# Kernel optimization log

Measured on AMD Instinct MI355X. Metric: run time of the kernel, lower is better.

The kernel has to match this reference:

```python
import jax, jax.numpy as jnp
import numpy as np

HIDDEN = 2048
NUM_EXPERTS = 64
TOP_K = 2
LOAD_BALANCE_ALPHA = 0.01
Z_LOSS_ALPHA = 1e-4
TEMPERATURE = 1.0  # buffer init, clamped to [0.1, 2.0] -> 1.0


def setup_inputs() -> dict:
    key = jax.random.key(0)
    k1, k2 = jax.random.split(key)
    x = jax.random.normal(k1, (4, 4096, HIDDEN), dtype=jnp.float32)
    W = jax.random.normal(k2, (NUM_EXPERTS, HIDDEN), dtype=jnp.float32) * (1.0 / np.sqrt(HIDDEN))
    return {"x": x, "W": W}


def reference(x, W):
    # Eval-mode forward of RuchbahMoEGate.
    B, S, H = x.shape
    x_flat = x.reshape(-1, H)                       # [N, H], N = B*S
    logits = jnp.einsum('nh,eh->ne', x_flat, W)     # gate projection, [N, E]
    logits = logits / TEMPERATURE                   # temp clamped to [0.1,2.0]
    scores = jax.nn.softmax(logits, axis=-1)        # [N, E]
    # top-k routing (eval: dynamic top-k == top_k, no capacity limitation)
    top_scores, top_idx = jax.lax.top_k(scores, TOP_K)   # [N, K]
    top_scores = jax.nn.softmax(top_scores.astype(jnp.float32), axis=-1).astype(x.dtype)
    # load-balance loss (eval: total_routing_count == 0 -> basic term only)
    expert_load = scores.mean(axis=0)               # [E]
    ideal_load = 1.0 / NUM_EXPERTS
    lb_loss = LOAD_BALANCE_ALPHA * jnp.sum((expert_load - ideal_load) ** 2)
    # z-loss: penalize large logit logsumexp
    z_loss = Z_LOSS_ALPHA * jnp.mean(jax.nn.logsumexp(logits, axis=-1) ** 2)
    total_loss = lb_loss + z_loss
    return top_scores, top_idx, total_loss
```

## Files before the change

kernel.cpp:

```cpp
#include <hip/hip_runtime.h>
#include <cstdint>
#include <cstddef>

#define HDIM 2048
#define NEXP 64
#define HC   16
#define BTOK 128
#define GTHR 128
#define PX   132
#define PW   68
#define GATE_TOK 16

__global__ __launch_bounds__(GTHR) void moe_gemm(const float* __restrict__ x,
                                                 const float* __restrict__ W,
                                                 float* __restrict__ partial,
                                                 int N, int HS) {
  __shared__ __align__(16) float xt[2][HC][PX];
  __shared__ __align__(16) float wt[2][HC][PW];

  const int ntb   = N / BTOK;
  const int tb    = blockIdx.x % ntb;
  const int hsIdx = blockIdx.x / ntb;
  const int tok0  = tb * BTOK;
  const int h0    = hsIdx * HS;
  const int tid   = threadIdx.x;
  const int lane  = tid & 63;
  const int wid   = tid >> 6;
  const int xoff  = wid * 64 + (lane >> 3) * 8;
  const int e0    = (lane & 7) * 8;
  const int srow  = tid >> 2;
  const int sj    = (tid & 3) * 4;

  float acc[8][8];
#pragma unroll
  for (int t = 0; t < 8; ++t)
#pragma unroll
    for (int e = 0; e < 8; ++e) acc[t][e] = 0.f;

  float4 xr[4], wr[2];

#pragma unroll
  for (int i = 0; i < 4; ++i)
    xr[i] = *reinterpret_cast<const float4*>(&x[(size_t)(tok0 + srow + i * 32) * HDIM + h0 + sj]);
#pragma unroll
  for (int i = 0; i < 2; ++i)
    wr[i] = *reinterpret_cast<const float4*>(&W[(size_t)(srow + i * 32) * HDIM + h0 + sj]);
#pragma unroll
  for (int i = 0; i < 4; ++i) {
    const int r = srow + i * 32;
    xt[0][sj + 0][r] = xr[i].x; xt[0][sj + 1][r] = xr[i].y;
    xt[0][sj + 2][r] = xr[i].z; xt[0][sj + 3][r] = xr[i].w;
  }
#pragma unroll
  for (int i = 0; i < 2; ++i) {
    const int r = srow + i * 32;
    wt[0][sj + 0][r] = wr[i].x; wt[0][sj + 1][r] = wr[i].y;
    wt[0][sj + 2][r] = wr[i].z; wt[0][sj + 3][r] = wr[i].w;
  }
  __syncthreads();

  const int niter = HS / HC;
  int cur = 0;
  for (int c = 0; c < niter; ++c) {
    if (c + 1 < niter) {
      const int hb = h0 + (c + 1) * HC;
#pragma unroll
      for (int i = 0; i < 4; ++i)
        xr[i] = *reinterpret_cast<const float4*>(&x[(size_t)(tok0 + srow + i * 32) * HDIM + hb + sj]);
#pragma unroll
      for (int i = 0; i < 2; ++i)
        wr[i] = *reinterpret_cast<const float4*>(&W[(size_t)(srow + i * 32) * HDIM + hb + sj]);
    }
#pragma unroll
    for (int h = 0; h < HC; ++h) {
      const float4 a0 = *reinterpret_cast<const float4*>(&xt[cur][h][xoff]);
      const float4 a1 = *reinterpret_cast<const float4*>(&xt[cur][h][xoff + 4]);
      const float4 b0 = *reinterpret_cast<const float4*>(&wt[cur][h][e0]);
      const float4 b1 = *reinterpret_cast<const float4*>(&wt[cur][h][e0 + 4]);
      const float xs[8] = {a0.x, a0.y, a0.z, a0.w, a1.x, a1.y, a1.z, a1.w};
      const float wv[8] = {b0.x, b0.y, b0.z, b0.w, b1.x, b1.y, b1.z, b1.w};
#pragma unroll
      for (int t = 0; t < 8; ++t)
#pragma unroll
        for (int e = 0; e < 8; ++e)
          acc[t][e] = fmaf(xs[t], wv[e], acc[t][e]);
    }
    if (c + 1 < niter) {
      const int nx = cur ^ 1;
#pragma unroll
      for (int i = 0; i < 4; ++i) {
        const int r = srow + i * 32;
        xt[nx][sj + 0][r] = xr[i].x; xt[nx][sj + 1][r] = xr[i].y;
        xt[nx][sj + 2][r] = xr[i].z; xt[nx][sj + 3][r] = xr[i].w;
      }
#pragma unroll
      for (int i = 0; i < 2; ++i) {
        const int r = srow + i * 32;
        wt[nx][sj + 0][r] = wr[i].x; wt[nx][sj + 1][r] = wr[i].y;
        wt[nx][sj + 2][r] = wr[i].z; wt[nx][sj + 3][r] = wr[i].w;
      }
    }
    __syncthreads();
    cur ^= 1;
  }

  const size_t base = ((size_t)hsIdx * N + (tok0 + xoff)) * NEXP + e0;
#pragma unroll
  for (int t = 0; t < 8; ++t) {
    *reinterpret_cast<float4*>(&partial[base + (size_t)t * NEXP]) =
        make_float4(acc[t][0], acc[t][1], acc[t][2], acc[t][3]);
    *reinterpret_cast<float4*>(&partial[base + (size_t)t * NEXP + 4]) =
        make_float4(acc[t][4], acc[t][5], acc[t][6], acc[t][7]);
  }
}

template <int HSPLIT>
__global__ __launch_bounds__(256) void moe_gate(const float* __restrict__ partial,
                                                int N,
                                                float* __restrict__ outS,
                                                float* __restrict__ outI,
                                                float* __restrict__ esumP,
                                                float* __restrict__ lse2P) {
  __shared__ float es[4][NEXP];
  __shared__ float l2[4];
  const int tid  = threadIdx.x;
  const int lane = tid & 63;
  const int w    = tid >> 6;
  const int base = blockIdx.x * GATE_TOK + w * 4;

  float esum = 0.f, lse2 = 0.f;
#pragma unroll
  for (int tt = 0; tt < 4; ++tt) {
    const int t = base + tt;
    float logit = 0.f;
#pragma unroll
    for (int hs = 0; hs < HSPLIT; ++hs)
      logit += partial[((size_t)hs * N + t) * NEXP + lane];

    float m = logit;
#pragma unroll
    for (int d = 1; d < 64; d <<= 1) m = fmaxf(m, __shfl_xor(m, d));
    const float p = expf(logit - m);
    float s = p;
#pragma unroll
    for (int d = 1; d < 64; d <<= 1) s += __shfl_xor(s, d);
    const float score = p / s;

    float v1 = score; int i1 = lane;
#pragma unroll
    for (int d = 1; d < 64; d <<= 1) {
      const float pv = __shfl_xor(v1, d);
      const int   pi = __shfl_xor(i1, d);
      if (pv > v1 || (pv == v1 && pi < i1)) { v1 = pv; i1 = pi; }
    }
    float v2 = (lane == i1) ? -1.f : score; int i2 = lane;
#pragma unroll
    for (int d = 1; d < 64; d <<= 1) {
      const float pv = __shfl_xor(v2, d);
      const int   pi = __shfl_xor(i2, d);
      if (pv > v2 || (pv == v2 && pi < i2)) { v2 = pv; i2 = pi; }
    }

    if (lane == 0) {
      const float mx  = fmaxf(v1, v2);
      const float e1  = expf(v1 - mx), e2 = expf(v2 - mx);
      const float inv = 1.f / (e1 + e2);
      *reinterpret_cast<float2*>(&outS[2 * (size_t)t]) = make_float2(e1 * inv, e2 * inv);
      *reinterpret_cast<float2*>(&outI[2 * (size_t)t]) = make_float2((float)i1, (float)i2);
    }

    esum += score;
    const float lse = m + logf(s);
    lse2 += lse * lse;
  }

  es[w][lane] = esum;
  if (lane == 0) l2[w] = lse2;
  __syncthreads();
  if (tid < NEXP)
    esumP[(size_t)blockIdx.x * NEXP + tid] = es[0][tid] + es[1][tid] + es[2][tid] + es[3][tid];
  if (tid == 0)
    lse2P[blockIdx.x] = l2[0] + l2[1] + l2[2] + l2[3];
}

__global__ __launch_bounds__(256) void moe_loss(const float* __restrict__ esumP,
                                                const float* __restrict__ lse2P,
                                                float* __restrict__ outL,
                                                int N, int nb) {
  __shared__ float es[4][NEXP];
  __shared__ float l2s[4];
  const int tid = threadIdx.x, lane = tid & 63, w = tid >> 6;

  float acc = 0.f;
  for (int b = w; b < nb; b += 4) acc += esumP[(size_t)b * NEXP + lane];
  es[w][lane] = acc;

  float la = 0.f;
  for (int b = tid; b < nb; b += 256) la += lse2P[b];
#pragma unroll
  for (int d = 1; d < 64; d <<= 1) la += __shfl_xor(la, d);
  if (lane == 0) l2s[w] = la;
  __syncthreads();

  if (tid < NEXP) {
    const float tot  = es[0][tid] + es[1][tid] + es[2][tid] + es[3][tid];
    const float load = tot / (float)N;
    const float dv   = load - 1.0f / 64.0f;
    float q = dv * dv;
#pragma unroll
    for (int d = 1; d < 64; d <<= 1) q += __shfl_xor(q, d);
    if (tid == 0) {
      const float lseSum = l2s[0] + l2s[1] + l2s[2] + l2s[3];
      outL[0] = 0.01f * q + 1e-4f * (lseSum / (float)N);
    }
  }
}

extern "C" void kernel_launch(void* const* d_in, const int* in_sizes, int n_in,
                              void* d_out, int out_size, void* d_ws, size_t ws_size,
                              hipStream_t stream) {
  const float* x = (const float*)d_in[0];
  const float* W = (const float*)d_in[1];
  const int N  = in_sizes[0] / HDIM;
  const int GB = N / GATE_TOK;

  float* out  = (float*)d_out;
  float* outS = out;
  float* outI = out + (size_t)2 * N;
  float* outL = out + (size_t)4 * N;

  int hsplit = 1;
  for (int h = 8; h >= 1; h >>= 1) {
    const size_t need = (size_t)h * N * NEXP * sizeof(float)
                      + (size_t)GB * (NEXP + 1) * sizeof(float) + 256;
    if (ws_size >= need) { hsplit = h; break; }
  }
  const int HS = HDIM / hsplit;

  float* partial = (float*)d_ws;
  float* esumP   = (float*)((char*)d_ws + (size_t)hsplit * N * NEXP * sizeof(float));
  float* lse2P   = esumP + (size_t)GB * NEXP;

  const int ntb = N / BTOK;
  moe_gemm<<<dim3(ntb * hsplit), dim3(GTHR), 0, stream>>>(x, W, partial, N, HS);
  switch (hsplit) {
    case 8: moe_gate<8><<<dim3(GB), dim3(256), 0, stream>>>(partial, N, outS, outI, esumP, lse2P); break;
    case 4: moe_gate<4><<<dim3(GB), dim3(256), 0, stream>>>(partial, N, outS, outI, esumP, lse2P); break;
    case 2: moe_gate<2><<<dim3(GB), dim3(256), 0, stream>>>(partial, N, outS, outI, esumP, lse2P); break;
    default: moe_gate<1><<<dim3(GB), dim3(256), 0, stream>>>(partial, N, outS, outI, esumP, lse2P); break;
  }
  moe_loss<<<dim3(1), dim3(256), 0, stream>>>(esumP, lse2P, outL, N, GB);
}
```

Measured before the change: 300.7 us.

## Fuse gate GEMM with softmax/top-k routing in one kernel via in-block K-split

Replaces the separate GEMM kernel (which wrote per-split partial logits to workspace) and the gate kernel with a single fused kernel. Each 256-thread block handles 64 tokens, with warp pairs splitting the hidden dimension in half and reducing their partial logits through shared memory. Softmax, top-2 and the per-block loss partials are then computed in place, one thread per token. This removes the partial-logit round trip through global memory and one launch, at the cost of only N/64 blocks and larger shared memory use, which may limit occupancy.

```diff
diff --git a/kernel.cpp b/kernel.cpp
--- a/kernel.cpp
+++ b/kernel.cpp
@@ -1,216 +1,216 @@
 #include <hip/hip_runtime.h>
+#include <cmath>
 #include <cstdint>
 #include <cstddef>
 
-#define HDIM 2048
-#define NEXP 64
-#define HC   16
-#define BTOK 128
-#define GTHR 128
-#define PX   132
-#define PW   68
-#define GATE_TOK 16
-
-__global__ __launch_bounds__(GTHR) void moe_gemm(const float* __restrict__ x,
+#define HDIM  2048
+#define HHALF 1024
+#define HC    16
+#define NCHUNK (HHALF / HC)
+#define NEXP  64
+#define BTOK  64
+#define PL    68
+
+__global__ __launch_bounds__(256) void moe_fused(const float* __restrict__ x,
                                                  const float* __restrict__ W,
-                                                 float* __restrict__ partial,
-                                                 int N, int HS) {
-  __shared__ __align__(16) float xt[2][HC][PX];
-  __shared__ __align__(16) float wt[2][HC][PW];
-
-  const int ntb   = N / BTOK;
-  const int tb    = blockIdx.x % ntb;
-  const int hsIdx = blockIdx.x / ntb;
-  const int tok0  = tb * BTOK;
-  const int h0    = hsIdx * HS;
-  const int tid   = threadIdx.x;
-  const int lane  = tid & 63;
-  const int wid   = tid >> 6;
-  const int xoff  = wid * 64 + (lane >> 3) * 8;
-  const int e0    = (lane & 7) * 8;
-  const int srow  = tid >> 2;
-  const int sj    = (tid & 3) * 4;
-
-  float acc[8][8];
-#pragma unroll
-  for (int t = 0; t < 8; ++t)
-#pragma unroll
-    for (int e = 0; e < 8; ++e) acc[t][e] = 0.f;
-
-  float4 xr[4], wr[2];
-
-#pragma unroll
-  for (int i = 0; i < 4; ++i)
-    xr[i] = *reinterpret_cast<const float4*>(&x[(size_t)(tok0 + srow + i * 32) * HDIM + h0 + sj]);
-#pragma unroll
-  for (int i = 0; i < 2; ++i)
-    wr[i] = *reinterpret_cast<const float4*>(&W[(size_t)(srow + i * 32) * HDIM + h0 + sj]);
-#pragma unroll
-  for (int i = 0; i < 4; ++i) {
-    const int r = srow + i * 32;
-    xt[0][sj + 0][r] = xr[i].x; xt[0][sj + 1][r] = xr[i].y;
-    xt[0][sj + 2][r] = xr[i].z; xt[0][sj + 3][r] = xr[i].w;
-  }
-#pragma unroll
-  for (int i = 0; i < 2; ++i) {
-    const int r = srow + i * 32;
-    wt[0][sj + 0][r] = wr[i].x; wt[0][sj + 1][r] = wr[i].y;
-    wt[0][sj + 2][r] = wr[i].z; wt[0][sj + 3][r] = wr[i].w;
-  }
-  __syncthreads();
-
-  const int niter = HS / HC;
-  int cur = 0;
-  for (int c = 0; c < niter; ++c) {
-    if (c + 1 < niter) {
-      const int hb = h0 + (c + 1) * HC;
-#pragma unroll
-      for (int i = 0; i < 4; ++i)
-        xr[i] = *reinterpret_cast<const float4*>(&x[(size_t)(tok0 + srow + i * 32) * HDIM + hb + sj]);
-#pragma unroll
-      for (int i = 0; i < 2; ++i)
-        wr[i] = *reinterpret_cast<const float4*>(&W[(size_t)(srow + i * 32) * HDIM + hb + sj]);
-    }
-#pragma unroll
-    for (int h = 0; h < HC; ++h) {
-      const float4 a0 = *reinterpret_cast<const float4*>(&xt[cur][h][xoff]);
-      const float4 a1 = *reinterpret_cast<const float4*>(&xt[cur][h][xoff + 4]);
-      const float4 b0 = *reinterpret_cast<const float4*>(&wt[cur][h][e0]);
-      const float4 b1 = *reinterpret_cast<const float4*>(&wt[cur][h][e0 + 4]);
-      const float xs[8] = {a0.x, a0.y, a0.z, a0.w, a1.x, a1.y, a1.z, a1.w};
-      const float wv[8] = {b0.x, b0.y, b0.z, b0.w, b1.x, b1.y, b1.z, b1.w};
-#pragma unroll
-      for (int t = 0; t < 8; ++t)
-#pragma unroll
-        for (int e = 0; e < 8; ++e)
-          acc[t][e] = fmaf(xs[t], wv[e], acc[t][e]);
-    }
-    if (c + 1 < niter) {
-      const int nx = cur ^ 1;
-#pragma unroll
-      for (int i = 0; i < 4; ++i) {
-        const int r = srow + i * 32;
-        xt[nx][sj + 0][r] = xr[i].x; xt[nx][sj + 1][r] = xr[i].y;
-        xt[nx][sj + 2][r] = xr[i].z; xt[nx][sj + 3][r] = xr[i].w;
-      }
-#pragma unroll
-      for (int i = 0; i < 2; ++i) {
-        const int r = srow + i * 32;
-        wt[nx][sj + 0][r] = wr[i].x; wt[nx][sj + 1][r] = wr[i].y;
-        wt[nx][sj + 2][r] = wr[i].z; wt[nx][sj + 3][r] = wr[i].w;
-      }
-    }
-    __syncthreads();
-    cur ^= 1;
-  }
-
-  const size_t base = ((size_t)hsIdx * N + (tok0 + xoff)) * NEXP + e0;
-#pragma unroll
-  for (int t = 0; t < 8; ++t) {
-    *reinterpret_cast<float4*>(&partial[base + (size_t)t * NEXP]) =
-        make_float4(acc[t][0], acc[t][1], acc[t][2], acc[t][3]);
-    *reinterpret_cast<float4*>(&partial[base + (size_t)t * NEXP + 4]) =
-        make_float4(acc[t][4], acc[t][5], acc[t][6], acc[t][7]);
-  }
-}
-
-template <int HSPLIT>
-__global__ __launch_bounds__(256) void moe_gate(const float* __restrict__ partial,
-                                                int N,
-                                                float* __restrict__ outS,
-                                                float* __restrict__ outI,
-                                                float* __restrict__ esumP,
-                                                float* __restrict__ lse2P) {
-  __shared__ float es[4][NEXP];
-  __shared__ float l2[4];
+                                                 float* __restrict__ outS,
+                                                 float* __restrict__ outI,
+                                                 float* __restrict__ esumP,
+                                                 float* __restrict__ lse2P,
+                                                 int N) {
+  __shared__ __align__(16) float xt[2][2][HC][PL];
+  __shared__ __align__(16) float wt[2][2][HC][PL];
+  __shared__ __align__(16) float lg[BTOK][PL];
+  __shared__ float invS[BTOK];
+  __shared__ float lseL[BTOK];
+  __shared__ float esL[4][NEXP];
+
+  const int b    = blockIdx.x;
+  const int tok0 = b * BTOK;
   const int tid  = threadIdx.x;
   const int lane = tid & 63;
   const int w    = tid >> 6;
-  const int base = blockIdx.x * GATE_TOK + w * 4;
-
-  float esum = 0.f, lse2 = 0.f;
-#pragma unroll
-  for (int tt = 0; tt < 4; ++tt) {
-    const int t = base + tt;
-    float logit = 0.f;
-#pragma unroll
-    for (int hs = 0; hs < HSPLIT; ++hs)
-      logit += partial[((size_t)hs * N + t) * NEXP + lane];
-
-    float m = logit;
-#pragma unroll
-    for (int d = 1; d < 64; d <<= 1) m = fmaxf(m, __shfl_xor(m, d));
-    const float p = expf(logit - m);
-    float s = p;
-#pragma unroll
-    for (int d = 1; d < 64; d <<= 1) s += __shfl_xor(s, d);
-    const float score = p / s;
-
-    float v1 = score; int i1 = lane;
-#pragma unroll
-    for (int d = 1; d < 64; d <<= 1) {
-      const float pv = __shfl_xor(v1, d);
-      const int   pi = __shfl_xor(i1, d);
-      if (pv > v1 || (pv == v1 && pi < i1)) { v1 = pv; i1 = pi; }
-    }
-    float v2 = (lane == i1) ? -1.f : score; int i2 = lane;
-#pragma unroll
-    for (int d = 1; d < 64; d <<= 1) {
-      const float pv = __shfl_xor(v2, d);
-      const int   pi = __shfl_xor(i2, d);
-      if (pv > v2 || (pv == v2 && pi < i2)) { v2 = pv; i2 = pi; }
-    }
-
-    if (lane == 0) {
-      const float mx  = fmaxf(v1, v2);
-      const float e1  = expf(v1 - mx), e2 = expf(v2 - mx);
-      const float inv = 1.f / (e1 + e2);
-      *reinterpret_cast<float2*>(&outS[2 * (size_t)t]) = make_float2(e1 * inv, e2 * inv);
-      *reinterpret_cast<float2*>(&outI[2 * (size_t)t]) = make_float2((float)i1, (float)i2);
-    }
-
-    esum += score;
+  const int eh   = w & 1;
+  const int hh   = w >> 1;
+  const int tg   = lane >> 3;
+  const int eg   = lane & 7;
+  const int row  = tid >> 2;
+  const int cq   = tid & 3;
+
+  const float* xp = x + (size_t)(tok0 + row) * HDIM + cq * 4;
+  const float* wp = W + (size_t)row * HDIM + cq * 4;
+
+  float acc[8][4];
+#pragma unroll
+  for (int t = 0; t < 8; ++t)
+#pragma unroll
+    for (int e = 0; e < 4; ++e) acc[t][e] = 0.f;
+
+  {
+    const float4 x0 = *reinterpret_cast<const float4*>(xp);
+    const float4 x1 = *reinterpret_cast<const float4*>(xp + HHALF);
+    const float4 w0 = *reinterpret_cast<const float4*>(wp);
+    const float4 w1 = *reinterpret_cast<const float4*>(wp + HHALF);
+    const int cc = cq * 4;
+    xt[0][0][cc+0][row] = x0.x; xt[0][0][cc+1][row] = x0.y;
+    xt[0][0][cc+2][row] = x0.z; xt[0][0][cc+3][row] = x0.w;
+    xt[0][1][cc+0][row] = x1.x; xt[0][1][cc+1][row] = x1.y;
+    xt[0][1][cc+2][row] = x1.z; xt[0][1][cc+3][row] = x1.w;
+    wt[0][0][cc+0][row] = w0.x; wt[0][0][cc+1][row] = w0.y;
+    wt[0][0][cc+2][row] = w0.z; wt[0][0][cc+3][row] = w0.w;
+    wt[0][1][cc+0][row] = w1.x; wt[0][1][cc+1][row] = w1.y;
+    wt[0][1][cc+2][row] = w1.z; wt[0][1][cc+3][row] = w1.w;
+  }
+  __syncthreads();
+
+  const int trow = tg * 8;
+  const int ecol = (eh << 5) + (eg << 2);
+
+  int cur = 0;
+  for (int c = 0; c < NCHUNK; ++c) {
+    float4 x0, x1, w0, w1;
+    const bool more = (c + 1 < NCHUNK);
+    if (more) {
+      const int off = (c + 1) * HC;
+      x0 = *reinterpret_cast<const float4*>(xp + off);
+      x1 = *reinterpret_cast<const float4*>(xp + HHALF + off);
+      w0 = *reinterpret_cast<const float4*>(wp + off);
+      w1 = *reinterpret_cast<const float4*>(wp + HHALF + off);
+    }
+#pragma unroll
+    for (int h = 0; h < HC; ++h) {
+      const float4 a0 = *reinterpret_cast<const float4*>(&xt[cur][hh][h][trow]);
+      const float4 a1 = *reinterpret_cast<const float4*>(&xt[cur][hh][h][trow + 4]);
+      const float4 bv = *reinterpret_cast<const float4*>(&wt[cur][hh][h][ecol]);
+      const float xs[8] = {a0.x, a0.y, a0.z, a0.w, a1.x, a1.y, a1.z, a1.w};
+      const float wv[4] = {bv.x, bv.y, bv.z, bv.w};
+#pragma unroll
+      for (int t = 0; t < 8; ++t)
+#pragma unroll
+        for (int e = 0; e < 4; ++e)
+          acc[t][e] = fmaf(xs[t], wv[e], acc[t][e]);
+    }
+    if (more) {
+      const int nb = cur ^ 1, cc = cq * 4;
+      xt[nb][0][cc+0][row] = x0.x; xt[nb][0][cc+1][row] = x0.y;
+      xt[nb][0][cc+2][row] = x0.z; xt[nb][0][cc+3][row] = x0.w;
+      xt[nb][1][cc+0][row] = x1.x; xt[nb][1][cc+1][row] = x1.y;
+      xt[nb][1][cc+2][row] = x1.z; xt[nb][1][cc+3][row] = x1.w;
+      wt[nb][0][cc+0][row] = w0.x; wt[nb][0][cc+1][row] = w0.y;
+      wt[nb][0][cc+2][row] = w0.z; wt[nb][0][cc+3][row] = w0.w;
+      wt[nb][1][cc+0][row] = w1.x; wt[nb][1][cc+1][row] = w1.y;
+      wt[nb][1][cc+2][row] = w1.z; wt[nb][1][cc+3][row] = w1.w;
+    }
+    __syncthreads();
+    cur ^= 1;
+  }
+
+  if (hh == 0) {
+#pragma unroll
+    for (int t = 0; t < 8; ++t)
+      *reinterpret_cast<float4*>(&lg[trow + t][ecol]) =
+          make_float4(acc[t][0], acc[t][1], acc[t][2], acc[t][3]);
+  }
+  __syncthreads();
+  if (hh == 1) {
+#pragma unroll
+    for (int t = 0; t < 8; ++t) {
+      float4 cv = *reinterpret_cast<const float4*>(&lg[trow + t][ecol]);
+      cv.x += acc[t][0]; cv.y += acc[t][1]; cv.z += acc[t][2]; cv.w += acc[t][3];
+      *reinterpret_cast<float4*>(&lg[trow + t][ecol]) = cv;
+    }
+  }
+  __syncthreads();
+
+  if (lane < 16) {
+    const int t = w * 16 + lane;
+    float m = -INFINITY, v2 = -INFINITY;
+    int i1 = 0, i2 = 0;
+#pragma unroll
+    for (int e4 = 0; e4 < 16; ++e4) {
+      const float4 lv = *reinterpret_cast<const float4*>(&lg[t][e4 * 4]);
+      const float ls[4] = {lv.x, lv.y, lv.z, lv.w};
+#pragma unroll
+      for (int j = 0; j < 4; ++j) {
+        const float l = ls[j];
+        const int e = e4 * 4 + j;
+        if (l > m)       { v2 = m; i2 = i1; m = l; i1 = e; }
+        else if (l > v2) { v2 = l; i2 = e; }
+      }
+    }
+    float s = 0.f;
+#pragma unroll
+    for (int e4 = 0; e4 < 16; ++e4) {
+      float4 lv = *reinterpret_cast<const float4*>(&lg[t][e4 * 4]);
+      lv.x = expf(lv.x - m); s += lv.x;
+      lv.y = expf(lv.y - m); s += lv.y;
+      lv.z = expf(lv.z - m); s += lv.z;
+      lv.w = expf(lv.w - m); s += lv.w;
+      *reinterpret_cast<float4*>(&lg[t][e4 * 4]) = lv;
+    }
+    const float v1s = 1.f / s;
+    const float v2s = expf(v2 - m) / s;
+    const float mx  = fmaxf(v1s, v2s);
+    const float e1  = expf(v1s - mx), e2 = expf(v2s - mx);
+    const float inv = 1.f / (e1 + e2);
+    *reinterpret_cast<float2*>(&outS[2 * (size_t)(tok0 + t)]) = make_float2(e1 * inv, e2 * inv);
+    *reinterpret_cast<float2*>(&outI[2 * (size_t)(tok0 + t)]) = make_float2((float)i1, (float)i2);
+    invS[t] = v1s;
     const float lse = m + logf(s);
-    lse2 += lse * lse;
-  }
-
-  es[w][lane] = esum;
-  if (lane == 0) l2[w] = lse2;
-  __syncthreads();
-  if (tid < NEXP)
-    esumP[(size_t)blockIdx.x * NEXP + tid] = es[0][tid] + es[1][tid] + es[2][tid] + es[3][tid];
-  if (tid == 0)
-    lse2P[blockIdx.x] = l2[0] + l2[1] + l2[2] + l2[3];
+    lseL[t] = lse * lse;
+  }
+  __syncthreads();
+
+  float ea = 0.f;
+#pragma unroll
+  for (int i = 0; i < 16; ++i) {
+    const int t = w * 16 + i;
+    ea = fmaf(lg[t][lane], invS[t], ea);
+  }
+  esL[w][lane] = ea;
+  __syncthreads();
+  if (w == 0) {
+    const float tot = ((esL[0][lane] + esL[1][lane]) + esL[2][lane]) + esL[3][lane];
+    esumP[(size_t)b * NEXP + lane] = tot;
+  }
+  if (w == 1) {
+    float la = lseL[lane];
+#pragma unroll
+    for (int d = 1; d < 64; d <<= 1) la += __shfl_xor(la, d);
+    if (lane == 0) lse2P[b] = la;
+  }
 }
 
 __global__ __launch_bounds__(256) void moe_loss(const float* __restrict__ esumP,
                                                 const float* __restrict__ lse2P,
                                                 float* __restrict__ outL,
-                                                int N, int nb) {
-  __shared__ float es[4][NEXP];
-  __shared__ float l2s[4];
+                                                int N, int NB) {
+  __shared__ float es4[4][NEXP];
+  __shared__ float l4[4];
   const int tid = threadIdx.x, lane = tid & 63, w = tid >> 6;
 
-  float acc = 0.f;
-  for (int b = w; b < nb; b += 4) acc += esumP[(size_t)b * NEXP + lane];
-  es[w][lane] = acc;
+  const int seg = NB / 4;
+  float a = 0.f;
+  for (int i = 0; i < seg; ++i)
+    a += esumP[(size_t)(w * seg + i) * NEXP + lane];
+  es4[w][lane] = a;
 
   float la = 0.f;
-  for (int b = tid; b < nb; b += 256) la += lse2P[b];
+  for (int i = tid; i < NB; i += 256) la += lse2P[i];
 #pragma unroll
   for (int d = 1; d < 64; d <<= 1) la += __shfl_xor(la, d);
-  if (lane == 0) l2s[w] = la;
+  if (lane == 0) l4[w] = la;
   __syncthreads();
 
   if (tid < NEXP) {
-    const float tot  = es[0][tid] + es[1][tid] + es[2][tid] + es[3][tid];
+    const float tot  = ((es4[0][tid] + es4[1][tid]) + es4[2][tid]) + es4[3][tid];
     const float load = tot / (float)N;
     const float dv   = load - 1.0f / 64.0f;
     float q = dv * dv;
 #pragma unroll
     for (int d = 1; d < 64; d <<= 1) q += __shfl_xor(q, d);
     if (tid == 0) {
-      const float lseSum = l2s[0] + l2s[1] + l2s[2] + l2s[3];
+      const float lseSum = ((l4[0] + l4[1]) + l4[2]) + l4[3];
       outL[0] = 0.01f * q + 1e-4f * (lseSum / (float)N);
     }
   }
@@ -222,32 +222,16 @@
   const float* x = (const float*)d_in[0];
   const float* W = (const float*)d_in[1];
   const int N  = in_sizes[0] / HDIM;
-  const int GB = N / GATE_TOK;
+  const int NB = N / BTOK;
 
   float* out  = (float*)d_out;
   float* outS = out;
   float* outI = out + (size_t)2 * N;
   float* outL = out + (size_t)4 * N;
 
-  int hsplit = 1;
-  for (int h = 8; h >= 1; h >>= 1) {
-    const size_t need = (size_t)h * N * NEXP * sizeof(float)
-                      + (size_t)GB * (NEXP + 1) * sizeof(float) + 256;
-    if (ws_size >= need) { hsplit = h; break; }
-  }
-  const int HS = HDIM / hsplit;
-
-  float* partial = (float*)d_ws;
-  float* esumP   = (float*)((char*)d_ws + (size_t)hsplit * N * NEXP * sizeof(float));
-  float* lse2P   = esumP + (size_t)GB * NEXP;
-
-  const int ntb = N / BTOK;
-  moe_gemm<<<dim3(ntb * hsplit), dim3(GTHR), 0, stream>>>(x, W, partial, N, HS);
-  switch (hsplit) {
-    case 8: moe_gate<8><<<dim3(GB), dim3(256), 0, stream>>>(partial, N, outS, outI, esumP, lse2P); break;
-    case 4: moe_gate<4><<<dim3(GB), dim3(256), 0, stream>>>(partial, N, outS, outI, esumP, lse2P); break;
-    case 2: moe_gate<2><<<dim3(GB), dim3(256), 0, stream>>>(partial, N, outS, outI, esumP, lse2P); break;
-    default: moe_gate<1><<<dim3(GB), dim3(256), 0, stream>>>(partial, N, outS, outI, esumP, lse2P); break;
-  }
-  moe_loss<<<dim3(1), dim3(256), 0, stream>>>(esumP, lse2P, outL, N, GB);
+  float* esumP = (float*)d_ws;
+  float* lse2P = esumP + (size_t)NB * NEXP;
+
+  moe_fused<<<dim3(NB), dim3(256), 0, stream>>>(x, W, outS, outI, esumP, lse2P, N);
+  moe_loss<<<dim3(1), dim3(256), 0, stream>>>(esumP, lse2P, outL, N, NB);
 }
```

Result: faster. 256.0 us (-14.9%).
